# Kernel optimization log

Hardware: AMD Instinct MI355X
Metric: run time of the kernel (lower is better)

The kernel has to match this reference:

```python
import jax, jax.numpy as jnp
import numpy as np

WS = (7, 7)  # window size
NUM_HEADS = 16


def _relative_position_index(ws):
    # Deterministic int index table, computed exactly as in the torch module.
    coords = np.stack(np.meshgrid(np.arange(ws[0]), np.arange(ws[1]), indexing='ij'))  # [2,Wh,Ww]
    coords = coords.reshape(2, -1)                       # [2, N]
    rel = coords[:, :, None] - coords[:, None, :]        # [2, N, N]
    rel = rel.transpose(1, 2, 0)                         # [N, N, 2]
    rel = rel + np.array([ws[0] - 1, ws[1] - 1])
    rel[:, :, 0] *= 2 * ws[1] - 1
    return jnp.asarray(rel.sum(-1), dtype=jnp.int32)     # [N, N]


def setup_inputs() -> dict:
    key = jax.random.key(0)
    ks = jax.random.split(key, 5)
    B_, N, C = 2048, WS[0] * WS[1], 512
    nw = 64
    return {
        'x': jax.random.normal(ks[0], (B_, N, C), dtype=jnp.float32),
        'mask': jax.random.normal(ks[1], (nw, N, N), dtype=jnp.float32),
        'qkv_w': jax.random.normal(ks[2], (3 * C, C), dtype=jnp.float32) * 0.02,
        'qkv_b': jax.random.normal(ks[3], (3 * C,), dtype=jnp.float32) * 0.02,
        'rpb_table': jax.random.normal(ks[4], ((2 * WS[0] - 1) * (2 * WS[1] - 1), NUM_HEADS), dtype=jnp.float32) * 0.02,
    }


def reference(x, mask, qkv_w, qkv_b, rpb_table):
    B_, N, C = x.shape
    H = NUM_HEADS
    hd = C // H
    scale = hd ** -0.5

    # qkv projection: [B_, N, 3, H, hd] -> q, k, v each [B_, H, N, hd]
    qkv = (jnp.einsum('bnc,oc->bno', x, qkv_w) + qkv_b)
    qkv = qkv.reshape(B_, N, 3, H, hd).transpose(2, 0, 3, 1, 4)
    q, k, v = qkv[0], qkv[1], qkv[2]

    attn = jnp.einsum('bhnd,bhmd->bhnm', q * scale, k)  # [B_, H, N, N]

    rel_idx = _relative_position_index(WS)                       # [N, N]
    bias = rpb_table[rel_idx.reshape(-1)].reshape(N, N, H)       # gather
    attn = attn + bias.transpose(2, 0, 1)[None]                  # [1, H, N, N]

    nw = mask.shape[0]
    attn = attn.reshape(B_ // nw, nw, H, N, N) + mask[None, :, None]
    attn = attn.reshape(B_, H, N, N)
    attn = jax.nn.softmax(attn, axis=-1)

    out = jnp.einsum('bhnm,bhmd->bhnd', attn, v)
    out = out.transpose(0, 2, 1, 3).reshape(B_, N, C)
    # NOTE: source assigns `X = self.proj(x)` but returns `x`, so the
    # output projection is dead code; we faithfully return pre-proj output.
    return out
```

## Files before the change

### kernel.cpp

```cpp
#include <hip/hip_runtime.h>
#include <cstdint>
#include <cstddef>

typedef __bf16 bf16x8 __attribute__((ext_vector_type(8)));
typedef float f32x4 __attribute__((ext_vector_type(4)));
typedef unsigned short u16x8 __attribute__((ext_vector_type(8)));

#define VT_LD 56
#define LDE 144

__device__ __forceinline__ unsigned short f2bf(float f) {
  unsigned int u = __builtin_bit_cast(unsigned int, f);
  u += 0x7FFFu + ((u >> 16) & 1u);
  return (unsigned short)(u >> 16);
}

__device__ __forceinline__ void gload_lds16(const void* g, void* l) {
  __builtin_amdgcn_global_load_lds((const __attribute__((address_space(1))) void*)g,
                                   (__attribute__((address_space(3))) void*)l, 16, 0, 0);
}

__global__ void conv_f2b_k(const float* __restrict__ src, unsigned short* __restrict__ dst, long n8) {
  long i = (long)blockIdx.x * blockDim.x + threadIdx.x;
  long stride = (long)gridDim.x * blockDim.x;
  for (; i < n8; i += stride) {
    float4 a = *(const float4*)(src + i * 8);
    float4 b = *(const float4*)(src + i * 8 + 4);
    u16x8 p;
    p[0]=f2bf(a.x); p[1]=f2bf(a.y); p[2]=f2bf(a.z); p[3]=f2bf(a.w);
    p[4]=f2bf(b.x); p[5]=f2bf(b.y); p[6]=f2bf(b.z); p[7]=f2bf(b.w);
    *(u16x8*)(dst + i * 8) = p;
  }
}

__global__ void build_bias_k(const float* __restrict__ rpb, float* __restrict__ biasT) {
  int idx = blockIdx.x * 256 + threadIdx.x;
  if (idx >= 16 * 2401) return;
  int h = idx / 2401;
  int rem = idx - h * 2401;
  int i = rem / 49, j = rem - (rem / 49) * 49;
  int r1 = i / 7, c1 = i - r1 * 7;
  int r2 = j / 7, c2 = j - r2 * 7;
  int ri = (r1 - r2 + 6) * 13 + (c1 - c2 + 6);
  biasT[idx] = rpb[ri * 16 + h];
}

__global__ __launch_bounds__(256, 3) void qkv_gemm_k(
    const unsigned short* __restrict__ xb, const float* __restrict__ qkv_b,
    const unsigned short* __restrict__ wb,
    unsigned short* __restrict__ qs, unsigned short* __restrict__ kk,
    unsigned short* __restrict__ vt)
{
  __shared__ __align__(16) unsigned short smem[18432];
  unsigned short* Ab = smem;
  unsigned short* Bb = smem + 4096;

  int bid = blockIdx.x;
  int sw = (bid & 7) * 1176 + (bid >> 3);
  int mt = sw / 12, nt = sw - mt * 12;
  long m0 = (long)mt * 128;
  int  n0 = nt * 128;
  int  s  = n0 >> 9;

  int t = threadIdx.x;
  int lane = t & 63, wv = t >> 6;
  int g = lane >> 4, q = lane & 15;
  int wrow = wv >> 1, wcol = wv & 1;

  f32x4 acc[4][4] = {};

  int schunk = (t & 3) ^ ((t >> 3) & 3);
  const unsigned short* ag0 = xb + (m0 + (t >> 2)) * 512 + schunk * 8;
  const unsigned short* ag1 = ag0 + 64 * 512;
  unsigned short* al0 = Ab + wv * 512;
  unsigned short* al1 = Ab + 2048 + wv * 512;
  const unsigned short* bg0 = wb + (size_t)(n0 + (t >> 2)) * 512 + schunk * 8;
  const unsigned short* bg1 = bg0 + 64 * 512;
  unsigned short* bl0 = Bb + wv * 512;
  unsigned short* bl1 = Bb + 2048 + wv * 512;

  int roff = (8 * g) ^ (((q >> 1) & 3) << 3);
  const unsigned short* ab = Ab + (wrow * 64 + q) * 32 + roff;
  const unsigned short* bb = Bb + (wcol * 64 + q) * 32 + roff;

  for (int kt = 0; kt < 16; ++kt) {
    int k0 = kt * 32;
    gload_lds16(ag0 + k0, al0);
    gload_lds16(ag1 + k0, al1);
    gload_lds16(bg0 + k0, bl0);
    gload_lds16(bg1 + k0, bl1);
    __syncthreads();

    bf16x8 af[4], bfr[4];
    #pragma unroll
    for (int i2 = 0; i2 < 4; ++i2) af[i2]  = *(const bf16x8*)(ab + i2 * 512);
    #pragma unroll
    for (int i2 = 0; i2 < 4; ++i2) bfr[i2] = *(const bf16x8*)(bb + i2 * 512);
    #pragma unroll
    for (int i2 = 0; i2 < 4; ++i2)
      #pragma unroll
      for (int j2 = 0; j2 < 4; ++j2)
        acc[i2][j2] = __builtin_amdgcn_mfma_f32_16x16x32_bf16(af[i2], bfr[j2], acc[i2][j2], 0, 0, 0);
    __syncthreads();
  }

  int   nl[4];
  float bias[4];
  #pragma unroll
  for (int j2 = 0; j2 < 4; ++j2) {
    nl[j2] = wcol * 64 + j2 * 16 + q;
    bias[j2] = qkv_b[n0 + nl[j2]];
  }

  if (s < 2) {
    float sc = (s == 0) ? 0.17677669529663687f : 1.0f;
    #pragma unroll
    for (int i2 = 0; i2 < 4; ++i2) {
      #pragma unroll
      for (int r = 0; r < 4; ++r) {
        int ml = wrow * 64 + i2 * 16 + 4 * g + r;
        #pragma unroll
        for (int j2 = 0; j2 < 4; ++j2)
          smem[ml * LDE + nl[j2]] = f2bf((acc[i2][j2][r] + bias[j2]) * sc);
      }
    }
    __syncthreads();
    unsigned short* dst = (s == 0) ? qs : kk;
    int c8 = (t & 15) * 8;
    int d0 = c8 & 31;
    int h  = ((n0 + c8) >> 5) & 15;
    #pragma unroll
    for (int p = 0; p < 8; ++p) {
      int row = p * 16 + (t >> 4);
      unsigned int gm = (unsigned int)m0 + row;
      unsigned int b  = gm / 49;
      unsigned int i  = gm - b * 49;
      u16x8 val = *(const u16x8*)(smem + row * LDE + c8);
      *(u16x8*)(dst + ((size_t)(b * 16 + h) * 49 + i) * 32 + d0) = val;
    }
  } else {
    #pragma unroll
    for (int j2 = 0; j2 < 4; ++j2) {
      int d = nl[j2] & 31;
      int h = ((n0 + nl[j2]) >> 5) & 15;
      #pragma unroll
      for (int i2 = 0; i2 < 4; ++i2) {
        unsigned int gm0 = (unsigned int)m0 + wrow * 64 + i2 * 16 + 4 * g;
        unsigned int b0 = gm0 / 49;
        unsigned int i0 = gm0 - b0 * 49;
        unsigned short hv[4];
        #pragma unroll
        for (int r = 0; r < 4; ++r) hv[r] = f2bf(acc[i2][j2][r] + bias[j2]);
        if (i0 <= 45) {
          unsigned short* base = vt + ((size_t)(b0 * 16 + h) * 32 + d) * VT_LD;
          if ((i0 & 1) == 0) {
            *(unsigned int*)(base + i0)     = (unsigned int)hv[0] | ((unsigned int)hv[1] << 16);
            *(unsigned int*)(base + i0 + 2) = (unsigned int)hv[2] | ((unsigned int)hv[3] << 16);
          } else {
            base[i0] = hv[0];
            *(unsigned int*)(base + i0 + 1) = (unsigned int)hv[1] | ((unsigned int)hv[2] << 16);
            base[i0 + 3] = hv[3];
          }
        } else {
          #pragma unroll
          for (int r = 0; r < 4; ++r) {
            unsigned int gm = gm0 + r;
            unsigned int b = gm / 49;
            unsigned int i = gm - b * 49;
            vt[((size_t)(b * 16 + h) * 32 + d) * VT_LD + i] = hv[r];
          }
        }
      }
    }
  }
}

__global__ __launch_bounds__(256, 2) void win_attn_k(
    const unsigned short* __restrict__ qs, const unsigned short* __restrict__ kk,
    const unsigned short* __restrict__ vt, const float* __restrict__ biasT,
    const float* __restrict__ mask, float* __restrict__ out)
{
  __shared__ float mlds[49 * 49];
  __shared__ unsigned short plds[4][64 * 72];

  int b = blockIdx.x;
  int t = threadIdx.x;
  int lane = t & 63, wv = t >> 6;
  int g = lane >> 4, q = lane & 15;

  const float* msrc = mask + (size_t)(b & 63) * 2401;
  for (int idx = t; idx < 2401; idx += 256) mlds[idx] = msrc[idx];
  __syncthreads();

  unsigned short* pl = plds[wv];

  for (int hh = 0; hh < 4; ++hh) {
    int h = wv * 4 + hh;
    const unsigned short* qh = qs + (size_t)(b * 16 + h) * (49 * 32);
    const unsigned short* kh = kk + (size_t)(b * 16 + h) * (49 * 32);
    const unsigned short* vh = vt + (size_t)(b * 16 + h) * (32 * VT_LD);
    const float* bhp = biasT + h * 2401;

    bf16x8 aq[4], bk[4];
    #pragma unroll
    for (int it = 0; it < 4; ++it) {
      int row = it * 16 + q; row = row > 48 ? 48 : row;
      aq[it] = *(const bf16x8*)(qh + row * 32 + 8 * g);
    }
    #pragma unroll
    for (int jt = 0; jt < 4; ++jt) {
      int row = jt * 16 + q; row = row > 48 ? 48 : row;
      bk[jt] = *(const bf16x8*)(kh + row * 32 + 8 * g);
    }
    f32x4 zero = {0.f, 0.f, 0.f, 0.f};
    f32x4 st[4][4];
    __builtin_amdgcn_s_setprio(1);
    #pragma unroll
    for (int it = 0; it < 4; ++it)
      #pragma unroll
      for (int jt = 0; jt < 4; ++jt)
        st[it][jt] = __builtin_amdgcn_mfma_f32_16x16x32_bf16(aq[it], bk[jt], zero, 0, 0, 0);
    __builtin_amdgcn_s_setprio(0);

    float rinv[4][4];
    #pragma unroll
    for (int it = 0; it < 4; ++it) {
      #pragma unroll
      for (int r = 0; r < 4; ++r) {
        int i = it * 16 + 4 * g + r;
        int ic = i > 48 ? 48 : i;
        float vj[4];
        #pragma unroll
        for (int jt = 0; jt < 4; ++jt) {
          int j = jt * 16 + q;
          float val;
          if (j < 49) val = st[it][jt][r] + bhp[ic * 49 + j] + mlds[ic * 49 + j];
          else        val = -__builtin_inff();
          vj[jt] = val;
        }
        float mx = fmaxf(fmaxf(vj[0], vj[1]), fmaxf(vj[2], vj[3]));
        #pragma unroll
        for (int off = 1; off < 16; off <<= 1) mx = fmaxf(mx, __shfl_xor(mx, off));
        float sm = 0.f;
        #pragma unroll
        for (int jt = 0; jt < 4; ++jt) {
          float p = __expf(vj[jt] - mx);
          st[it][jt][r] = p;
          sm += p;
        }
        #pragma unroll
        for (int off = 1; off < 16; off <<= 1) sm += __shfl_xor(sm, off);
        rinv[it][r] = 1.0f / sm;
      }
    }

    #pragma unroll
    for (int it = 0; it < 4; ++it)
      #pragma unroll
      for (int jt = 0; jt < 4; ++jt)
        #pragma unroll
        for (int r = 0; r < 4; ++r) {
          int i = it * 16 + 4 * g + r;
          int j = jt * 16 + q;
          pl[i * 72 + j] = f2bf(st[it][jt][r]);
        }

    f32x4 oacc[4][2] = {};
    #pragma unroll
    for (int ktt = 0; ktt < 2; ++ktt) {
      bf16x8 pa[4], bv[2];
      #pragma unroll
      for (int it = 0; it < 4; ++it)
        pa[it] = *(const bf16x8*)(pl + (it * 16 + q) * 72 + ktt * 32 + 8 * g);
      #pragma unroll
      for (int dt = 0; dt < 2; ++dt)
        bv[dt] = *(const bf16x8*)(vh + (dt * 16 + q) * VT_LD + ktt * 32 + 8 * g);
      __builtin_amdgcn_s_setprio(1);
      #pragma unroll
      for (int it = 0; it < 4; ++it)
        #pragma unroll
        for (int dt = 0; dt < 2; ++dt)
          oacc[it][dt] = __builtin_amdgcn_mfma_f32_16x16x32_bf16(pa[it], bv[dt], oacc[it][dt], 0, 0, 0);
      __builtin_amdgcn_s_setprio(0);
    }

    #pragma unroll
    for (int it = 0; it < 4; ++it) {
      #pragma unroll
      for (int dt = 0; dt < 2; ++dt) {
        #pragma unroll
        for (int r = 0; r < 4; ++r) {
          int i = it * 16 + 4 * g + r;
          if (i < 49) {
            int d = dt * 16 + q;
            out[(size_t)(b * 49 + i) * 512 + h * 32 + d] = oacc[it][dt][r] * rinv[it][r];
          }
        }
      }
    }
  }
}

extern "C" void kernel_launch(void* const* d_in, const int* in_sizes, int n_in,
                              void* d_out, int out_size, void* d_ws, size_t ws_size,
                              hipStream_t stream) {
  const float* x     = (const float*)d_in[0];
  const float* mask  = (const float*)d_in[1];
  const float* qkv_w = (const float*)d_in[2];
  const float* qkv_b = (const float*)d_in[3];
  const float* rpb   = (const float*)d_in[4];
  float* out = (float*)d_out;

  const size_t QS_OFF   = 0;
  const size_t KK_OFF   = 102760448;
  const size_t VT_OFF   = 205520896;
  const size_t BIAS_OFF = 322961408;
  const size_t WB_OFF   = 323115072;
  const size_t NEED     = 324687936;
  if (ws_size < NEED) return;

  char* ws = (char*)d_ws;
  unsigned short* qsb   = (unsigned short*)(ws + QS_OFF);
  unsigned short* kkb   = (unsigned short*)(ws + KK_OFF);
  unsigned short* vtb   = (unsigned short*)(ws + VT_OFF);
  float*          biasT = (float*)(ws + BIAS_OFF);
  unsigned short* wb    = (unsigned short*)(ws + WB_OFF);

  unsigned short* xb = (unsigned short*)d_out;

  conv_f2b_k<<<2048, 256, 0, stream>>>(x, xb, 6422528);
  conv_f2b_k<<<512, 256, 0, stream>>>(qkv_w, wb, 98304);
  build_bias_k<<<151, 256, 0, stream>>>(rpb, biasT);
  qkv_gemm_k<<<9408, 256, 0, stream>>>(xb, qkv_b, wb, qsb, kkb, vtb);
  win_attn_k<<<2048, 256, 0, stream>>>(qsb, kkb, vtb, biasT, mask, out);
}
```

Measured before the change: 510.4 us.

## Double K-step per barrier in QKV GEMM and raise attention occupancy

The QKV projection GEMM now loads a 64-wide K slab (two 32-wide panels) per iteration using 8 async global-to-LDS loads per thread, halving the number of loop iterations and __syncthreads barriers. The loop is fully unrolled and the load mapping is reorganised per wave with a matching XOR swizzle. The float-to-bf16 helper switches to the compiler's native conversion, and the attention kernel's launch bounds ask for 3 blocks per CU instead of 2, which may force register spilling.

New measurement: 648.9 us. 27.1% more time.

```diff
diff --git a/kernel.cpp b/kernel.cpp
--- a/kernel.cpp
+++ b/kernel.cpp
@@ -10,9 +10,8 @@
 #define LDE 144
 
 __device__ __forceinline__ unsigned short f2bf(float f) {
-  unsigned int u = __builtin_bit_cast(unsigned int, f);
-  u += 0x7FFFu + ((u >> 16) & 1u);
-  return (unsigned short)(u >> 16);
+  __bf16 h = (__bf16)f;
+  return __builtin_bit_cast(unsigned short, h);
 }
 
 __device__ __forceinline__ void gload_lds16(const void* g, void* l) {
@@ -53,7 +52,7 @@
 {
   __shared__ __align__(16) unsigned short smem[18432];
   unsigned short* Ab = smem;
-  unsigned short* Bb = smem + 4096;
+  unsigned short* Bb = smem + 8192;
 
   int bid = blockIdx.x;
   int sw = (bid & 7) * 1176 + (bid >> 3);
@@ -69,33 +68,53 @@
 
   f32x4 acc[4][4] = {};
 
-  int schunk = (t & 3) ^ ((t >> 3) & 3);
-  const unsigned short* ag0 = xb + (m0 + (t >> 2)) * 512 + schunk * 8;
-  const unsigned short* ag1 = ag0 + 64 * 512;
-  unsigned short* al0 = Ab + wv * 512;
-  unsigned short* al1 = Ab + 2048 + wv * 512;
-  const unsigned short* bg0 = wb + (size_t)(n0 + (t >> 2)) * 512 + schunk * 8;
-  const unsigned short* bg1 = bg0 + 64 * 512;
-  unsigned short* bl0 = Bb + wv * 512;
-  unsigned short* bl1 = Bb + 2048 + wv * 512;
-
-  int roff = (8 * g) ^ (((q >> 1) & 3) << 3);
-  const unsigned short* ab = Ab + (wrow * 64 + q) * 32 + roff;
-  const unsigned short* bb = Bb + (wcol * 64 + q) * 32 + roff;
-
-  for (int kt = 0; kt < 16; ++kt) {
-    int k0 = kt * 32;
-    gload_lds16(ag0 + k0, al0);
-    gload_lds16(ag1 + k0, al1);
-    gload_lds16(bg0 + k0, bl0);
-    gload_lds16(bg1 + k0, bl1);
+  int cg = (lane & 3) ^ ((lane >> 3) & 3);
+  int lrow = lane >> 2;
+  const unsigned short* agp[4];
+  const unsigned short* bgp[4];
+  unsigned short* alb[4];
+  unsigned short* blb[4];
+  #pragma unroll
+  for (int c = 0; c < 4; ++c) {
+    int ci = wv * 4 + c;
+    int p = ci >> 3, rg = ci & 7;
+    int row = rg * 16 + lrow;
+    agp[c] = xb + (m0 + row) * 512 + p * 32 + cg * 8;
+    bgp[c] = wb + (size_t)(n0 + row) * 512 + p * 32 + cg * 8;
+    alb[c] = Ab + ci * 512;
+    blb[c] = Bb + ci * 512;
+  }
+
+  int csw = (g ^ ((q >> 1) & 3)) * 8;
+  const unsigned short* ar0 = Ab + (wrow * 64 + q) * 32 + csw;
+  const unsigned short* ar1 = ar0 + 4096;
+  const unsigned short* br0 = Bb + (wcol * 64 + q) * 32 + csw;
+  const unsigned short* br1 = br0 + 4096;
+
+  #pragma unroll
+  for (int kt = 0; kt < 8; ++kt) {
+    int k0 = kt * 64;
+    #pragma unroll
+    for (int c = 0; c < 4; ++c) {
+      gload_lds16(agp[c] + k0, alb[c]);
+      gload_lds16(bgp[c] + k0, blb[c]);
+    }
     __syncthreads();
 
     bf16x8 af[4], bfr[4];
     #pragma unroll
-    for (int i2 = 0; i2 < 4; ++i2) af[i2]  = *(const bf16x8*)(ab + i2 * 512);
-    #pragma unroll
-    for (int i2 = 0; i2 < 4; ++i2) bfr[i2] = *(const bf16x8*)(bb + i2 * 512);
+    for (int i2 = 0; i2 < 4; ++i2) af[i2]  = *(const bf16x8*)(ar0 + i2 * 512);
+    #pragma unroll
+    for (int j2 = 0; j2 < 4; ++j2) bfr[j2] = *(const bf16x8*)(br0 + j2 * 512);
+    #pragma unroll
+    for (int i2 = 0; i2 < 4; ++i2)
+      #pragma unroll
+      for (int j2 = 0; j2 < 4; ++j2)
+        acc[i2][j2] = __builtin_amdgcn_mfma_f32_16x16x32_bf16(af[i2], bfr[j2], acc[i2][j2], 0, 0, 0);
+    #pragma unroll
+    for (int i2 = 0; i2 < 4; ++i2) af[i2]  = *(const bf16x8*)(ar1 + i2 * 512);
+    #pragma unroll
+    for (int j2 = 0; j2 < 4; ++j2) bfr[j2] = *(const bf16x8*)(br1 + j2 * 512);
     #pragma unroll
     for (int i2 = 0; i2 < 4; ++i2)
       #pragma unroll
@@ -175,7 +194,7 @@
   }
 }
 
-__global__ __launch_bounds__(256, 2) void win_attn_k(
+__global__ __launch_bounds__(256, 3) void win_attn_k(
     const unsigned short* __restrict__ qs, const unsigned short* __restrict__ kk,
     const unsigned short* __restrict__ vt, const float* __restrict__ biasT,
     const float* __restrict__ mask, float* __restrict__ out)
```
